# Kernel tuning notes

Hardware: AMD Instinct MI355X
Metric: run time of the kernel (lower is better)

Reference implementation:

```python
import jax, jax.numpy as jnp
from jax import lax
import numpy as np

# ---- module hyper-params (from init_kwargs) ----
ANCHORS = np.array([[42.0, 45.0], [98.0, 130.0], [180.0, 260.0],
                    [300.0, 180.0], [400.0, 400.0]], dtype=np.float32)  # (A,2) pixels
STRIDE = 32
NUM_CLASSES = 80
A = ANCHORS.shape[0]
IMG_H, IMG_W = 1024, 1024  # decode img_size
BN_EPS = 1e-5
TW_CLAMP_MAX = 8.0


def setup_inputs() -> dict:
    key = jax.random.key(0)
    ks = jax.random.split(key, 8)
    B, Cin, S = 32, 512, 32
    Cout = A * (5 + NUM_CLASSES)  # 425
    return {
        "features": jax.random.normal(ks[0], (B, Cin, S, S), jnp.float32),
        "conv1_w": jax.random.normal(ks[1], (1024, Cin, 3, 3), jnp.float32) * 0.02,
        "bn_gamma": jax.random.uniform(ks[2], (1024,), jnp.float32, 0.5, 1.5),
        "bn_beta": jax.random.normal(ks[3], (1024,), jnp.float32) * 0.1,
        "bn_mean": jax.random.normal(ks[4], (1024,), jnp.float32) * 0.1,
        "bn_var": jax.random.uniform(ks[5], (1024,), jnp.float32, 0.5, 1.5),
        "conv2_w": jax.random.normal(ks[6], (Cout, 1024, 1, 1), jnp.float32) * 0.02,
        "conv2_b": jax.random.normal(ks[7], (Cout,), jnp.float32) * 0.02,
    }


def _conv_pred(features, conv1_w, bn_gamma, bn_beta, bn_mean, bn_var, conv2_w, conv2_b):
    dn = ("NCHW", "OIHW", "NCHW")
    x = lax.conv_general_dilated(features, conv1_w, (1, 1), ((1, 1), (1, 1)),
                                 dimension_numbers=dn)
    # BatchNorm (eval mode) fused with LeakyReLU(0.1)
    scale = bn_gamma / jnp.sqrt(bn_var + BN_EPS)
    x = x * scale[None, :, None, None] + (bn_beta - bn_mean * scale)[None, :, None, None]
    x = jnp.where(x > 0, x, 0.1 * x)
    p = lax.conv_general_dilated(x, conv2_w, (1, 1), ((0, 0), (0, 0)),
                                 dimension_numbers=dn)
    p = p + conv2_b[None, :, None, None]
    # (B, A*(5+C), Sy, Sx) -> (B, Sy, Sx, A*(5+C))
    return jnp.transpose(p, (0, 2, 3, 1))


def _decode(preds):
    B, Sy, Sx, _ = preds.shape
    C = NUM_CLASSES
    p = preds.reshape(B, Sy, Sx, A, 5 + C)
    tx, ty, tw, th, to = p[..., 0], p[..., 1], p[..., 2], p[..., 3], p[..., 4]
    cls_logits = p[..., 5:]

    bx = jax.nn.sigmoid(tx)
    by = jax.nn.sigmoid(ty)
    bw = jnp.exp(jnp.minimum(tw, TW_CLAMP_MAX))
    bh = jnp.exp(jnp.minimum(th, TW_CLAMP_MAX))
    obj = jax.nn.sigmoid(to)
    cls_prob = jax.nn.softmax(cls_logits, axis=-1)

    grid_y = jnp.arange(Sy, dtype=preds.dtype)[None, :, None, None]  # (1,Sy,1,1)
    grid_x = jnp.arange(Sx, dtype=preds.dtype)[None, None, :, None]  # (1,1,Sx,1)
    anc = jnp.asarray(ANCHORS) / STRIDE  # cell units
    anc_w = anc[:, 0][None, None, None, :]
    anc_h = anc[:, 1][None, None, None, :]

    cx = (bx + grid_x) * STRIDE
    cy = (by + grid_y) * STRIDE
    pw = anc_w * bw * STRIDE
    ph = anc_h * bh * STRIDE

    x1 = jnp.clip(cx - pw * 0.5, 0.0, IMG_W - 1)
    y1 = jnp.clip(cy - ph * 0.5, 0.0, IMG_H - 1)
    x2 = jnp.clip(cx + pw * 0.5, 0.0, IMG_W - 1)
    y2 = jnp.clip(cy + ph * 0.5, 0.0, IMG_H - 1)

    boxes = jnp.stack((x1, y1, x2, y2), axis=-1).reshape(B, -1, 4)  # (B, Sy*Sx*A, 4)
    scores = (obj * jnp.max(cls_prob, axis=-1)).reshape(B, -1)       # (B, Sy*Sx*A)
    labels = jnp.argmax(cls_prob, axis=-1).reshape(B, -1)            # (B, Sy*Sx*A)
    out5 = jnp.concatenate([boxes, scores[..., None]], axis=-1)      # (B, N, 5)
    return out5, labels


def reference(features, conv1_w, bn_gamma, bn_beta, bn_mean, bn_var, conv2_w, conv2_b):
    preds = _conv_pred(features, conv1_w, bn_gamma, bn_beta, bn_mean, bn_var,
                       conv2_w, conv2_b)
    out5, labels = _decode(preds)
    return out5, labels
```

## Files before the change

### kernel.cpp

```cpp
#include <hip/hip_runtime.h>


typedef _Float16 f16;
typedef _Float16 f16x8 __attribute__((ext_vector_type(8)));
typedef _Float16 f16x4v __attribute__((ext_vector_type(4)));
typedef float    f32x4 __attribute__((ext_vector_type(4)));

__device__ __forceinline__ void gload16(const f16* g, f16* l) {
  __builtin_amdgcn_global_load_lds(
      (const __attribute__((address_space(1))) void*)g,
      (__attribute__((address_space(3))) void*)l, 16, 0, 0);
}

#define MFMA(a, b, c) __builtin_amdgcn_mfma_f32_16x16x32_f16(a, b, c, 0, 0, 0)
#define ASM_VMCNT(N) asm volatile("s_waitcnt vmcnt(" #N ")" ::: "memory")
#define SBAR()                           \
  {                                      \
    __builtin_amdgcn_s_barrier();        \
    __builtin_amdgcn_sched_barrier(0);   \
  }

#define R_AH 0
#define R_AL 16384
#define R_BH 32768
#define R_BL 49152

__device__ const float c_AW[5] = {42.f, 98.f, 180.f, 300.f, 400.f};
__device__ const float c_AH_[5] = {45.f, 130.f, 260.f, 180.f, 400.f};

__global__ void prep_misc(const float* __restrict__ g, const float* __restrict__ be,
                          const float* __restrict__ mn, const float* __restrict__ vr,
                          const float* __restrict__ b2,
                          float* __restrict__ scale, float* __restrict__ shift,
                          float* __restrict__ bias) {
  int i = threadIdx.x;
  float s = g[i] / sqrtf(vr[i] + 1e-5f);
  shift[i] = be[i] - mn[i] * s;
  scale[i] = s * (1.0f / 1024.0f);
  if (i < 512) bias[i] = (i < 425) ? b2[i] : 0.f;
}

__global__ __launch_bounds__(256) void prep_w1(const float* __restrict__ w,
                                               f16* __restrict__ Ah, f16* __restrict__ Al) {
  const int co = blockIdx.x;
  const int k = blockIdx.y * 256 + threadIdx.x;
  const int ky = k / 1536, rem = k - ky * 1536;
  const int kx = rem >> 9, ci = rem & 511;
  float v = w[((co * 512 + ci) * 3 + ky) * 3 + kx] * 1024.f;
  f16 h = (f16)v;
  Ah[(long)co * 4608 + k] = h;
  Al[(long)co * 4608 + k] = (f16)(v - (float)h);
}

__global__ __launch_bounds__(256) void prep_w2(const float* __restrict__ w,
                                               f16* __restrict__ Ah, f16* __restrict__ Al) {
  const int co = blockIdx.x;
  const int ci = blockIdx.y * 256 + threadIdx.x;
  float v = (co < 425) ? w[co * 1024 + ci] * 1024.f : 0.f;
  f16 h = (f16)v;
  Ah[co * 1024 + ci] = h;
  Al[co * 1024 + ci] = (f16)(v - (float)h);
}

__global__ __launch_bounds__(256) void prep_feat(const float* __restrict__ f,
                                                 f16* __restrict__ fph, f16* __restrict__ fpl) {
  __shared__ float lds[256][33];
  const int y = blockIdx.x, b = blockIdx.y, t = threadIdx.x;
  const int xx = t & 31, cig = t >> 5;
  const float* src = f + ((long)b * 512) * 1024 + y * 32;

  for (int half = 0; half < 2; ++half) {
    const int cibase = half * 256;
    for (int rep = 0; rep < 32; ++rep) {
      int ci = rep * 8 + cig;
      lds[ci][xx] = src[(long)(cibase + ci) * 1024 + xx];
    }
    __syncthreads();
    const long rowbase = ((long)(b * 34) + (y + 1)) * 34 + 1;
    for (int xp = 0; xp < 32; ++xp) {
      float v = lds[t][xp];
      f16 h = (f16)v;
      long o = (rowbase + xp) * 512 + cibase + t;
      fph[o] = h;
      fpl[o] = (f16)(v - (float)h);
    }
    __syncthreads();
  }
}

__global__ __launch_bounds__(512, 2) void gemm1(
    const f16* __restrict__ A1h, const f16* __restrict__ A1l,
    const f16* __restrict__ Bh, const f16* __restrict__ Bl,
    const float* __restrict__ scale, const float* __restrict__ shift,
    f16* __restrict__ xth, f16* __restrict__ xtl) {
  __shared__ __align__(16) f16 S[65536];
  const int tid = threadIdx.x;
  const int l = tid & 63, w = tid >> 6;
  const int wm = w >> 2, wn = w & 3;
  const int rho = l & 15, cq = l >> 4;
  const int sc = (cq - rho) & 3;
  const int roff = (rho + 16 * ((cq + rho) & 3)) * 8;
  const int nt = blockIdx.x, mt = blockIdx.y;
  const int n0 = nt * 256, co0 = mt * 256;
  const int b = n0 >> 10, y0 = (n0 & 1023) >> 5;

  const int a0u = (w & 3) + (w >> 2) * 8;
  const int a1u = a0u + 4;
  const int b0u = (w & 1) + (w >> 1) * 4;
  const int b1u = b0u + 2;

  const long aS0 = (long)(co0 + a0u * 16 + rho) * 4608 + sc * 8;
  const long aS1 = (long)(co0 + a1u * 16 + rho) * 4608 + sc * 8;
  const int c0 = b0u * 16 + rho, c1 = b1u * 16 + rho;
  const long bS0 = ((long)(b * 34 + y0 + (c0 >> 5)) * 34 + (c0 & 31)) * 512 + sc * 8;
  const long bS1 = ((long)(b * 34 + y0 + (c1 >> 5)) * 34 + (c1 & 31)) * 512 + sc * 8;

  f32x4 acc[8][4] = {};
  f16x8 ah[4], al[4], bh[2], bl[2];

  gload16(A1h + aS0, &S[R_AH + a0u * 512]);
  gload16(A1l + aS0, &S[R_AL + a0u * 512]);
  gload16(Bh + bS0, &S[R_BH + b0u * 512]);
  gload16(Bl + bS0, &S[R_BL + b0u * 512]);
  gload16(A1h + aS1, &S[R_AH + a1u * 512]);
  gload16(A1l + aS1, &S[R_AL + a1u * 512]);
  gload16(Bh + bS1, &S[R_BH + b1u * 512]);
  gload16(Bl + bS1, &S[R_BL + b1u * 512]);
  ASM_VMCNT(4);
  SBAR();

  for (int t = 0; t < 144; ++t) {
    const int cb = (t & 1) << 13;
    const int nb = 8192 - cb;
    const int s1 = (t < 143) ? t + 1 : t;
    const int ky1 = s1 / 48, r1 = s1 - ky1 * 48;
    const int kx1 = r1 >> 4, ci1 = (r1 & 15) << 5;
    const long kAn = (long)s1 * 32;
    const long kBn = (long)(ky1 * 34 + kx1) * 512 + ci1;

#pragma unroll
    for (int mf = 0; mf < 4; ++mf) {
      const int u = wm * 8 + mf;
      ah[mf] = *(const f16x8*)&S[R_AH + cb + u * 512 + roff];
      al[mf] = *(const f16x8*)&S[R_AL + cb + u * 512 + roff];
    }
#pragma unroll
    for (int nf = 0; nf < 2; ++nf) {
      const int u = wn * 4 + nf;
      bh[nf] = *(const f16x8*)&S[R_BH + cb + u * 512 + roff];
      bl[nf] = *(const f16x8*)&S[R_BL + cb + u * 512 + roff];
    }
    gload16(A1h + aS0 + kAn, &S[R_AH + nb + a0u * 512]);
    gload16(A1l + aS0 + kAn, &S[R_AL + nb + a0u * 512]);
    ASM_VMCNT(2);
    SBAR();
    __builtin_amdgcn_s_setprio(1);
#pragma unroll
    for (int mf = 0; mf < 4; ++mf)
#pragma unroll
      for (int nf = 0; nf < 2; ++nf) {
        acc[mf][nf] = MFMA(ah[mf], bh[nf], acc[mf][nf]);
        acc[mf][nf] = MFMA(ah[mf], bl[nf], acc[mf][nf]);
        acc[mf][nf] = MFMA(al[mf], bh[nf], acc[mf][nf]);
      }
    __builtin_amdgcn_s_setprio(0);
    SBAR();

#pragma unroll
    for (int nf = 0; nf < 2; ++nf) {
      const int u = wn * 4 + 2 + nf;
      bh[nf] = *(const f16x8*)&S[R_BH + cb + u * 512 + roff];
      bl[nf] = *(const f16x8*)&S[R_BL + cb + u * 512 + roff];
    }
    gload16(Bh + bS0 + kBn, &S[R_BH + nb + b0u * 512]);
    gload16(Bl + bS0 + kBn, &S[R_BL + nb + b0u * 512]);
    SBAR();
    __builtin_amdgcn_s_setprio(1);
#pragma unroll
    for (int mf = 0; mf < 4; ++mf)
#pragma unroll
      for (int nf = 0; nf < 2; ++nf) {
        acc[mf][2 + nf] = MFMA(ah[mf], bh[nf], acc[mf][2 + nf]);
        acc[mf][2 + nf] = MFMA(ah[mf], bl[nf], acc[mf][2 + nf]);
        acc[mf][2 + nf] = MFMA(al[mf], bh[nf], acc[mf][2 + nf]);
      }
    __builtin_amdgcn_s_setprio(0);
    SBAR();

#pragma unroll
    for (int mf = 0; mf < 4; ++mf) {
      const int u = wm * 8 + 4 + mf;
      ah[mf] = *(const f16x8*)&S[R_AH + cb + u * 512 + roff];
      al[mf] = *(const f16x8*)&S[R_AL + cb + u * 512 + roff];
    }
#pragma unroll
    for (int nf = 0; nf < 2; ++nf) {
      const int u = wn * 4 + nf;
      bh[nf] = *(const f16x8*)&S[R_BH + cb + u * 512 + roff];
      bl[nf] = *(const f16x8*)&S[R_BL + cb + u * 512 + roff];
    }
    gload16(A1h + aS1 + kAn, &S[R_AH + nb + a1u * 512]);
    gload16(A1l + aS1 + kAn, &S[R_AL + nb + a1u * 512]);
    SBAR();
    __builtin_amdgcn_s_setprio(1);
#pragma unroll
    for (int mf = 0; mf < 4; ++mf)
#pragma unroll
      for (int nf = 0; nf < 2; ++nf) {
        acc[4 + mf][nf] = MFMA(ah[mf], bh[nf], acc[4 + mf][nf]);
        acc[4 + mf][nf] = MFMA(ah[mf], bl[nf], acc[4 + mf][nf]);
        acc[4 + mf][nf] = MFMA(al[mf], bh[nf], acc[4 + mf][nf]);
      }
    __builtin_amdgcn_s_setprio(0);
    SBAR();

#pragma unroll
    for (int nf = 0; nf < 2; ++nf) {
      const int u = wn * 4 + 2 + nf;
      bh[nf] = *(const f16x8*)&S[R_BH + cb + u * 512 + roff];
      bl[nf] = *(const f16x8*)&S[R_BL + cb + u * 512 + roff];
    }
    gload16(Bh + bS1 + kBn, &S[R_BH + nb + b1u * 512]);
    gload16(Bl + bS1 + kBn, &S[R_BL + nb + b1u * 512]);
    ASM_VMCNT(4);
    SBAR();
    __builtin_amdgcn_s_setprio(1);
#pragma unroll
    for (int mf = 0; mf < 4; ++mf)
#pragma unroll
      for (int nf = 0; nf < 2; ++nf) {
        acc[4 + mf][2 + nf] = MFMA(ah[mf], bh[nf], acc[4 + mf][2 + nf]);
        acc[4 + mf][2 + nf] = MFMA(ah[mf], bl[nf], acc[4 + mf][2 + nf]);
        acc[4 + mf][2 + nf] = MFMA(al[mf], bh[nf], acc[4 + mf][2 + nf]);
      }
    __builtin_amdgcn_s_setprio(0);
    SBAR();
  }

#pragma unroll
  for (int am = 0; am < 8; ++am) {
    const int cob = co0 + wm * 128 + am * 16 + cq * 4;
    const float4 scv = *(const float4*)(scale + cob);
    const float4 shv = *(const float4*)(shift + cob);
#pragma unroll
    for (int an = 0; an < 4; ++an) {
      const int col = n0 + wn * 64 + an * 16 + rho;
      f32x4 a = acc[am][an];
      float v0 = a[0] * scv.x + shv.x; v0 = v0 > 0.f ? v0 : 0.1f * v0;
      float v1 = a[1] * scv.y + shv.y; v1 = v1 > 0.f ? v1 : 0.1f * v1;
      float v2 = a[2] * scv.z + shv.z; v2 = v2 > 0.f ? v2 : 0.1f * v2;
      float v3 = a[3] * scv.w + shv.w; v3 = v3 > 0.f ? v3 : 0.1f * v3;
      f16 h0 = (f16)v0, h1 = (f16)v1, h2 = (f16)v2, h3 = (f16)v3;
      f16x4v hv = {h0, h1, h2, h3};
      f16x4v lv = {(f16)(v0 - (float)h0), (f16)(v1 - (float)h1),
                   (f16)(v2 - (float)h2), (f16)(v3 - (float)h3)};
      *(f16x4v*)(xth + (long)col * 1024 + cob) = hv;
      *(f16x4v*)(xtl + (long)col * 1024 + cob) = lv;
    }
  }
}

__global__ __launch_bounds__(512, 2) void gemm2(
    const f16* __restrict__ A2h, const f16* __restrict__ A2l,
    const f16* __restrict__ Bh, const f16* __restrict__ Bl,
    const float* __restrict__ bias, float* __restrict__ preds) {
  __shared__ __align__(16) f16 S[65536];
  const int tid = threadIdx.x;
  const int l = tid & 63, w = tid >> 6;
  const int wm = w >> 2, wn = w & 3;
  const int rho = l & 15, cq = l >> 4;
  const int sc = (cq - rho) & 3;
  const int roff = (rho + 16 * ((cq + rho) & 3)) * 8;
  const int nt = blockIdx.x, mt = blockIdx.y;
  const int n0 = nt * 256, co0 = mt * 256;

  const int a0u = (w & 3) + (w >> 2) * 8;
  const int a1u = a0u + 4;
  const int b0u = (w & 1) + (w >> 1) * 4;
  const int b1u = b0u + 2;

  const long aS0 = (long)(co0 + a0u * 16 + rho) * 1024 + sc * 8;
  const long aS1 = (long)(co0 + a1u * 16 + rho) * 1024 + sc * 8;
  const long bS0 = (long)(n0 + b0u * 16 + rho) * 1024 + sc * 8;
  const long bS1 = (long)(n0 + b1u * 16 + rho) * 1024 + sc * 8;

  f32x4 acc[8][4] = {};
  f16x8 ah[4], al[4], bh[2], bl[2];

  gload16(A2h + aS0, &S[R_AH + a0u * 512]);
  gload16(A2l + aS0, &S[R_AL + a0u * 512]);
  gload16(Bh + bS0, &S[R_BH + b0u * 512]);
  gload16(Bl + bS0, &S[R_BL + b0u * 512]);
  gload16(A2h + aS1, &S[R_AH + a1u * 512]);
  gload16(A2l + aS1, &S[R_AL + a1u * 512]);
  gload16(Bh + bS1, &S[R_BH + b1u * 512]);
  gload16(Bl + bS1, &S[R_BL + b1u * 512]);
  ASM_VMCNT(4);
  SBAR();

  for (int t = 0; t < 32; ++t) {
    const int cb = (t & 1) << 13;
    const int nb = 8192 - cb;
    const long kn = (long)((t < 31) ? t + 1 : t) * 32;

#pragma unroll
    for (int mf = 0; mf < 4; ++mf) {
      const int u = wm * 8 + mf;
      ah[mf] = *(const f16x8*)&S[R_AH + cb + u * 512 + roff];
      al[mf] = *(const f16x8*)&S[R_AL + cb + u * 512 + roff];
    }
#pragma unroll
    for (int nf = 0; nf < 2; ++nf) {
      const int u = wn * 4 + nf;
      bh[nf] = *(const f16x8*)&S[R_BH + cb + u * 512 + roff];
      bl[nf] = *(const f16x8*)&S[R_BL + cb + u * 512 + roff];
    }
    gload16(A2h + aS0 + kn, &S[R_AH + nb + a0u * 512]);
    gload16(A2l + aS0 + kn, &S[R_AL + nb + a0u * 512]);
    ASM_VMCNT(2);
    SBAR();
    __builtin_amdgcn_s_setprio(1);
#pragma unroll
    for (int mf = 0; mf < 4; ++mf)
#pragma unroll
      for (int nf = 0; nf < 2; ++nf) {
        acc[mf][nf] = MFMA(ah[mf], bh[nf], acc[mf][nf]);
        acc[mf][nf] = MFMA(ah[mf], bl[nf], acc[mf][nf]);
        acc[mf][nf] = MFMA(al[mf], bh[nf], acc[mf][nf]);
      }
    __builtin_amdgcn_s_setprio(0);
    SBAR();

#pragma unroll
    for (int nf = 0; nf < 2; ++nf) {
      const int u = wn * 4 + 2 + nf;
      bh[nf] = *(const f16x8*)&S[R_BH + cb + u * 512 + roff];
      bl[nf] = *(const f16x8*)&S[R_BL + cb + u * 512 + roff];
    }
    gload16(Bh + bS0 + kn, &S[R_BH + nb + b0u * 512]);
    gload16(Bl + bS0 + kn, &S[R_BL + nb + b0u * 512]);
    SBAR();
    __builtin_amdgcn_s_setprio(1);
#pragma unroll
    for (int mf = 0; mf < 4; ++mf)
#pragma unroll
      for (int nf = 0; nf < 2; ++nf) {
        acc[mf][2 + nf] = MFMA(ah[mf], bh[nf], acc[mf][2 + nf]);
        acc[mf][2 + nf] = MFMA(ah[mf], bl[nf], acc[mf][2 + nf]);
        acc[mf][2 + nf] = MFMA(al[mf], bh[nf], acc[mf][2 + nf]);
      }
    __builtin_amdgcn_s_setprio(0);
    SBAR();

#pragma unroll
    for (int mf = 0; mf < 4; ++mf) {
      const int u = wm * 8 + 4 + mf;
      ah[mf] = *(const f16x8*)&S[R_AH + cb + u * 512 + roff];
      al[mf] = *(const f16x8*)&S[R_AL + cb + u * 512 + roff];
    }
#pragma unroll
    for (int nf = 0; nf < 2; ++nf) {
      const int u = wn * 4 + nf;
      bh[nf] = *(const f16x8*)&S[R_BH + cb + u * 512 + roff];
      bl[nf] = *(const f16x8*)&S[R_BL + cb + u * 512 + roff];
    }
    gload16(A2h + aS1 + kn, &S[R_AH + nb + a1u * 512]);
    gload16(A2l + aS1 + kn, &S[R_AL + nb + a1u * 512]);
    SBAR();
    __builtin_amdgcn_s_setprio(1);
#pragma unroll
    for (int mf = 0; mf < 4; ++mf)
#pragma unroll
      for (int nf = 0; nf < 2; ++nf) {
        acc[4 + mf][nf] = MFMA(ah[mf], bh[nf], acc[4 + mf][nf]);
        acc[4 + mf][nf] = MFMA(ah[mf], bl[nf], acc[4 + mf][nf]);
        acc[4 + mf][nf] = MFMA(al[mf], bh[nf], acc[4 + mf][nf]);
      }
    __builtin_amdgcn_s_setprio(0);
    SBAR();

#pragma unroll
    for (int nf = 0; nf < 2; ++nf) {
      const int u = wn * 4 + 2 + nf;
      bh[nf] = *(const f16x8*)&S[R_BH + cb + u * 512 + roff];
      bl[nf] = *(const f16x8*)&S[R_BL + cb + u * 512 + roff];
    }
    gload16(Bh + bS1 + kn, &S[R_BH + nb + b1u * 512]);
    gload16(Bl + bS1 + kn, &S[R_BL + nb + b1u * 512]);
    ASM_VMCNT(4);
    SBAR();
    __builtin_amdgcn_s_setprio(1);
#pragma unroll
    for (int mf = 0; mf < 4; ++mf)
#pragma unroll
      for (int nf = 0; nf < 2; ++nf) {
        acc[4 + mf][2 + nf] = MFMA(ah[mf], bh[nf], acc[4 + mf][2 + nf]);
        acc[4 + mf][2 + nf] = MFMA(ah[mf], bl[nf], acc[4 + mf][2 + nf]);
        acc[4 + mf][2 + nf] = MFMA(al[mf], bh[nf], acc[4 + mf][2 + nf]);
      }
    __builtin_amdgcn_s_setprio(0);
    SBAR();
  }

#pragma unroll
  for (int am = 0; am < 8; ++am) {
    const int cob = co0 + wm * 128 + am * 16 + cq * 4;
    const float4 bi = *(const float4*)(bias + cob);
#pragma unroll
    for (int an = 0; an < 4; ++an) {
      const int col = n0 + wn * 64 + an * 16 + rho;
      f32x4 a = acc[am][an];
      float4 o;
      o.x = a[0] * 9.765625e-4f + bi.x;
      o.y = a[1] * 9.765625e-4f + bi.y;
      o.z = a[2] * 9.765625e-4f + bi.z;
      o.w = a[3] * 9.765625e-4f + bi.w;
      *(float4*)(preds + (long)col * 512 + cob) = o;
    }
  }
}

__global__ __launch_bounds__(256) void decode(const float* __restrict__ preds,
                                              float* __restrict__ out) {
  const int t = blockIdx.x * 256 + threadIdx.x;
  const int b = t / 5120, rem = t % 5120, pos = rem / 5, a = rem % 5;
  const int n = (b << 10) + pos;
  const float* p = preds + (long)n * 512 + a * 85;

  float tx = p[0], ty = p[1], tw = p[2], th = p[3], to = p[4];
  float mx = p[5];
  int arg = 0;
  for (int i = 1; i < 80; ++i) {
    float v = p[5 + i];
    if (v > mx) { mx = v; arg = i; }
  }
  float sum = 0.f;
  for (int i = 0; i < 80; ++i) sum += expf(p[5 + i] - mx);

  float obj = 1.f / (1.f + expf(-to));
  float score = obj / sum;
  float bx = 1.f / (1.f + expf(-tx));
  float by = 1.f / (1.f + expf(-ty));
  float bw = expf(fminf(tw, 8.f));
  float bh2 = expf(fminf(th, 8.f));
  float cx = (bx + (float)(pos & 31)) * 32.f;
  float cy = (by + (float)(pos >> 5)) * 32.f;
  float pw = c_AW[a] * bw;
  float ph = c_AH_[a] * bh2;
  float x1 = fminf(fmaxf(cx - 0.5f * pw, 0.f), 1023.f);
  float y1 = fminf(fmaxf(cy - 0.5f * ph, 0.f), 1023.f);
  float x2 = fminf(fmaxf(cx + 0.5f * pw, 0.f), 1023.f);
  float y2 = fminf(fmaxf(cy + 0.5f * ph, 0.f), 1023.f);

  const long o = ((long)b * 5120 + pos * 5 + a) * 5;
  out[o + 0] = x1;
  out[o + 1] = y1;
  out[o + 2] = x2;
  out[o + 3] = y2;
  out[o + 4] = score;
  out[819200 + (long)b * 5120 + pos * 5 + a] = (float)arg;
}

extern "C" void kernel_launch(void* const* d_in, const int* in_sizes, int n_in,
                              void* d_out, int out_size, void* d_ws, size_t ws_size,
                              hipStream_t stream) {
  (void)in_sizes; (void)n_in; (void)out_size; (void)ws_size;
  const float* features = (const float*)d_in[0];
  const float* conv1_w = (const float*)d_in[1];
  const float* bn_g = (const float*)d_in[2];
  const float* bn_b = (const float*)d_in[3];
  const float* bn_m = (const float*)d_in[4];
  const float* bn_v = (const float*)d_in[5];
  const float* conv2_w = (const float*)d_in[6];
  const float* conv2_b = (const float*)d_in[7];
  float* out = (float*)d_out;
  char* ws = (char*)d_ws;

  f16* fph = (f16*)(ws + 0);
  f16* fpl = (f16*)(ws + 37879808L);
  f16* A1h = (f16*)(ws + 75759616L);
  f16* A1l = (f16*)(ws + 85196800L);
  f16* A2h = (f16*)(ws + 94633984L);
  f16* A2l = (f16*)(ws + 95682560L);
  float* scale = (float*)(ws + 96731136L);
  float* shift = (float*)(ws + 96735232L);
  float* bias = (float*)(ws + 96739328L);
  f16* xth = (f16*)(ws + 96741376L);
  f16* xtl = (f16*)(ws + 163850240L);
  float* preds = (float*)(ws + 0);

  hipMemsetAsync(ws, 0, 75759616L, stream);
  prep_misc<<<1, 1024, 0, stream>>>(bn_g, bn_b, bn_m, bn_v, conv2_b, scale, shift, bias);
  prep_w1<<<dim3(1024, 18), 256, 0, stream>>>(conv1_w, A1h, A1l);
  prep_w2<<<dim3(512, 4), 256, 0, stream>>>(conv2_w, A2h, A2l);
  prep_feat<<<dim3(32, 32), 256, 0, stream>>>(features, fph, fpl);
  gemm1<<<dim3(128, 4), 512, 0, stream>>>(A1h, A1l, fph, fpl, scale, shift, xth, xtl);
  gemm2<<<dim3(128, 2), 512, 0, stream>>>(A2h, A2l, xth, xtl, bias, preds);
  decode<<<640, 256, 0, stream>>>(preds, out);
}
```

Measured before the change: 930.1 us.

## Switch both GEMMs to 32x32x16 MFMA with restructured LDS staging

Both split-f16 GEMM kernels move from 16x16x32 MFMA tiles to 32x32x16 MFMA, with each warp now holding a 4x2 grid of 32x32 accumulators. The LDS tile layout is rebuilt to match: each wave loads a 32-row chunk split into two K-halves, the XOR-style swizzle offsets are dropped, and the pipeline goes from four sub-stages to two per K step. The goal is fewer LDS fragment reads per flop and higher MFMA throughput per instruction. Without the swizzle, LDS bank conflicts may rise, and the epilogue now follows the 32x32 output layout.

Result: slower. 1.148 ms (+23.4%).

```diff
diff --git a/kernel.cpp b/kernel.cpp
--- a/kernel.cpp
+++ b/kernel.cpp
@@ -4,7 +4,7 @@
 typedef _Float16 f16;
 typedef _Float16 f16x8 __attribute__((ext_vector_type(8)));
 typedef _Float16 f16x4v __attribute__((ext_vector_type(4)));
-typedef float    f32x4 __attribute__((ext_vector_type(4)));
+typedef float    f32x16 __attribute__((ext_vector_type(16)));
 
 __device__ __forceinline__ void gload16(const f16* g, f16* l) {
   __builtin_amdgcn_global_load_lds(
@@ -12,7 +12,7 @@
       (__attribute__((address_space(3))) void*)l, 16, 0, 0);
 }
 
-#define MFMA(a, b, c) __builtin_amdgcn_mfma_f32_16x16x32_f16(a, b, c, 0, 0, 0)
+#define MFMA32(a, b, c) __builtin_amdgcn_mfma_f32_32x32x16_f16(a, b, c, 0, 0, 0)
 #define ASM_VMCNT(N) asm volatile("s_waitcnt vmcnt(" #N ")" ::: "memory")
 #define SBAR()                           \
   {                                      \
@@ -97,165 +97,122 @@
   const int tid = threadIdx.x;
   const int l = tid & 63, w = tid >> 6;
   const int wm = w >> 2, wn = w & 3;
-  const int rho = l & 15, cq = l >> 4;
-  const int sc = (cq - rho) & 3;
-  const int roff = (rho + 16 * ((cq + rho) & 3)) * 8;
+  const int l31 = l & 31, lh = l >> 5;
   const int nt = blockIdx.x, mt = blockIdx.y;
   const int n0 = nt * 256, co0 = mt * 256;
   const int b = n0 >> 10, y0 = (n0 & 1023) >> 5;
 
-  const int a0u = (w & 3) + (w >> 2) * 8;
-  const int a1u = a0u + 4;
-  const int b0u = (w & 1) + (w >> 1) * 4;
-  const int b1u = b0u + 2;
-
-  const long aS0 = (long)(co0 + a0u * 16 + rho) * 4608 + sc * 8;
-  const long aS1 = (long)(co0 + a1u * 16 + rho) * 4608 + sc * 8;
-  const int c0 = b0u * 16 + rho, c1 = b1u * 16 + rho;
-  const long bS0 = ((long)(b * 34 + y0 + (c0 >> 5)) * 34 + (c0 & 31)) * 512 + sc * 8;
-  const long bS1 = ((long)(b * 34 + y0 + (c1 >> 5)) * 34 + (c1 & 31)) * 512 + sc * 8;
-
-  f32x4 acc[8][4] = {};
+  const long aSrc = (long)(co0 + 32 * w + l31) * 4608 + 8 * lh;
+  const long bSrc = ((long)(b * 34 + y0 + w) * 34 + l31) * 512 + 8 * lh;
+  const int dA = (w * 2) * 512;
+  const int lro = l * 8;
+
+  f32x16 acc[4][2] = {};
   f16x8 ah[4], al[4], bh[2], bl[2];
 
-  gload16(A1h + aS0, &S[R_AH + a0u * 512]);
-  gload16(A1l + aS0, &S[R_AL + a0u * 512]);
-  gload16(Bh + bS0, &S[R_BH + b0u * 512]);
-  gload16(Bl + bS0, &S[R_BL + b0u * 512]);
-  gload16(A1h + aS1, &S[R_AH + a1u * 512]);
-  gload16(A1l + aS1, &S[R_AL + a1u * 512]);
-  gload16(Bh + bS1, &S[R_BH + b1u * 512]);
-  gload16(Bl + bS1, &S[R_BL + b1u * 512]);
+  gload16(A1h + aSrc, &S[R_AH + dA]);
+  gload16(A1l + aSrc, &S[R_AL + dA]);
+  gload16(Bh + bSrc, &S[R_BH + dA]);
+  gload16(Bl + bSrc, &S[R_BL + dA]);
+  gload16(A1h + aSrc + 16, &S[R_AH + dA + 512]);
+  gload16(A1l + aSrc + 16, &S[R_AL + dA + 512]);
+  gload16(Bh + bSrc + 16, &S[R_BH + dA + 512]);
+  gload16(Bl + bSrc + 16, &S[R_BL + dA + 512]);
   ASM_VMCNT(4);
   SBAR();
 
   for (int t = 0; t < 144; ++t) {
     const int cb = (t & 1) << 13;
     const int nb = 8192 - cb;
-    const int s1 = (t < 143) ? t + 1 : t;
-    const int ky1 = s1 / 48, r1 = s1 - ky1 * 48;
+    const int s1t = (t < 143) ? t + 1 : t;
+    const int ky1 = s1t / 48, r1 = s1t - ky1 * 48;
     const int kx1 = r1 >> 4, ci1 = (r1 & 15) << 5;
-    const long kAn = (long)s1 * 32;
+    const long kAn = (long)s1t * 32;
     const long kBn = (long)(ky1 * 34 + kx1) * 512 + ci1;
 
+    gload16(A1h + aSrc + kAn, &S[R_AH + nb + dA]);
+    gload16(A1l + aSrc + kAn, &S[R_AL + nb + dA]);
+    gload16(Bh + bSrc + kBn, &S[R_BH + nb + dA]);
+    gload16(Bl + bSrc + kBn, &S[R_BL + nb + dA]);
 #pragma unroll
     for (int mf = 0; mf < 4; ++mf) {
-      const int u = wm * 8 + mf;
-      ah[mf] = *(const f16x8*)&S[R_AH + cb + u * 512 + roff];
-      al[mf] = *(const f16x8*)&S[R_AL + cb + u * 512 + roff];
-    }
-#pragma unroll
-    for (int nf = 0; nf < 2; ++nf) {
-      const int u = wn * 4 + nf;
-      bh[nf] = *(const f16x8*)&S[R_BH + cb + u * 512 + roff];
-      bl[nf] = *(const f16x8*)&S[R_BL + cb + u * 512 + roff];
-    }
-    gload16(A1h + aS0 + kAn, &S[R_AH + nb + a0u * 512]);
-    gload16(A1l + aS0 + kAn, &S[R_AL + nb + a0u * 512]);
-    ASM_VMCNT(2);
+      const int ch = ((wm * 4 + mf) * 2) * 512;
+      ah[mf] = *(const f16x8*)&S[R_AH + cb + ch + lro];
+      al[mf] = *(const f16x8*)&S[R_AL + cb + ch + lro];
+    }
+#pragma unroll
+    for (int nf = 0; nf < 2; ++nf) {
+      const int ch = ((wn * 2 + nf) * 2) * 512;
+      bh[nf] = *(const f16x8*)&S[R_BH + cb + ch + lro];
+      bl[nf] = *(const f16x8*)&S[R_BL + cb + ch + lro];
+    }
+    ASM_VMCNT(4);
     SBAR();
     __builtin_amdgcn_s_setprio(1);
 #pragma unroll
     for (int mf = 0; mf < 4; ++mf)
 #pragma unroll
       for (int nf = 0; nf < 2; ++nf) {
-        acc[mf][nf] = MFMA(ah[mf], bh[nf], acc[mf][nf]);
-        acc[mf][nf] = MFMA(ah[mf], bl[nf], acc[mf][nf]);
-        acc[mf][nf] = MFMA(al[mf], bh[nf], acc[mf][nf]);
+        acc[mf][nf] = MFMA32(ah[mf], bh[nf], acc[mf][nf]);
+        acc[mf][nf] = MFMA32(ah[mf], bl[nf], acc[mf][nf]);
+        acc[mf][nf] = MFMA32(al[mf], bh[nf], acc[mf][nf]);
       }
     __builtin_amdgcn_s_setprio(0);
     SBAR();
 
-#pragma unroll
-    for (int nf = 0; nf < 2; ++nf) {
-      const int u = wn * 4 + 2 + nf;
-      bh[nf] = *(const f16x8*)&S[R_BH + cb + u * 512 + roff];
-      bl[nf] = *(const f16x8*)&S[R_BL + cb + u * 512 + roff];
-    }
-    gload16(Bh + bS0 + kBn, &S[R_BH + nb + b0u * 512]);
-    gload16(Bl + bS0 + kBn, &S[R_BL + nb + b0u * 512]);
+    gload16(A1h + aSrc + kAn + 16, &S[R_AH + nb + dA + 512]);
+    gload16(A1l + aSrc + kAn + 16, &S[R_AL + nb + dA + 512]);
+    gload16(Bh + bSrc + kBn + 16, &S[R_BH + nb + dA + 512]);
+    gload16(Bl + bSrc + kBn + 16, &S[R_BL + nb + dA + 512]);
+#pragma unroll
+    for (int mf = 0; mf < 4; ++mf) {
+      const int ch = ((wm * 4 + mf) * 2 + 1) * 512;
+      ah[mf] = *(const f16x8*)&S[R_AH + cb + ch + lro];
+      al[mf] = *(const f16x8*)&S[R_AL + cb + ch + lro];
+    }
+#pragma unroll
+    for (int nf = 0; nf < 2; ++nf) {
+      const int ch = ((wn * 2 + nf) * 2 + 1) * 512;
+      bh[nf] = *(const f16x8*)&S[R_BH + cb + ch + lro];
+      bl[nf] = *(const f16x8*)&S[R_BL + cb + ch + lro];
+    }
+    ASM_VMCNT(4);
     SBAR();
     __builtin_amdgcn_s_setprio(1);
 #pragma unroll
     for (int mf = 0; mf < 4; ++mf)
 #pragma unroll
       for (int nf = 0; nf < 2; ++nf) {
-        acc[mf][2 + nf] = MFMA(ah[mf], bh[nf], acc[mf][2 + nf]);
-        acc[mf][2 + nf] = MFMA(ah[mf], bl[nf], acc[mf][2 + nf]);
-        acc[mf][2 + nf] = MFMA(al[mf], bh[nf], acc[mf][2 + nf]);
+        acc[mf][nf] = MFMA32(ah[mf], bh[nf], acc[mf][nf]);
+        acc[mf][nf] = MFMA32(ah[mf], bl[nf], acc[mf][nf]);
+        acc[mf][nf] = MFMA32(al[mf], bh[nf], acc[mf][nf]);
       }
     __builtin_amdgcn_s_setprio(0);
     SBAR();
-
-#pragma unroll
-    for (int mf = 0; mf < 4; ++mf) {
-      const int u = wm * 8 + 4 + mf;
-      ah[mf] = *(const f16x8*)&S[R_AH + cb + u * 512 + roff];
-      al[mf] = *(const f16x8*)&S[R_AL + cb + u * 512 + roff];
-    }
-#pragma unroll
-    for (int nf = 0; nf < 2; ++nf) {
-      const int u = wn * 4 + nf;
-      bh[nf] = *(const f16x8*)&S[R_BH + cb + u * 512 + roff];
-      bl[nf] = *(const f16x8*)&S[R_BL + cb + u * 512 + roff];
-    }
-    gload16(A1h + aS1 + kAn, &S[R_AH + nb + a1u * 512]);
-    gload16(A1l + aS1 + kAn, &S[R_AL + nb + a1u * 512]);
-    SBAR();
-    __builtin_amdgcn_s_setprio(1);
-#pragma unroll
-    for (int mf = 0; mf < 4; ++mf)
-#pragma unroll
-      for (int nf = 0; nf < 2; ++nf) {
-        acc[4 + mf][nf] = MFMA(ah[mf], bh[nf], acc[4 + mf][nf]);
-        acc[4 + mf][nf] = MFMA(ah[mf], bl[nf], acc[4 + mf][nf]);
-        acc[4 + mf][nf] = MFMA(al[mf], bh[nf], acc[4 + mf][nf]);
-      }
-    __builtin_amdgcn_s_setprio(0);
-    SBAR();
-
-#pragma unroll
-    for (int nf = 0; nf < 2; ++nf) {
-      const int u = wn * 4 + 2 + nf;
-      bh[nf] = *(const f16x8*)&S[R_BH + cb + u * 512 + roff];
-      bl[nf] = *(const f16x8*)&S[R_BL + cb + u * 512 + roff];
-    }
-    gload16(Bh + bS1 + kBn, &S[R_BH + nb + b1u * 512]);
-    gload16(Bl + bS1 + kBn, &S[R_BL + nb + b1u * 512]);
-    ASM_VMCNT(4);
-    SBAR();
-    __builtin_amdgcn_s_setprio(1);
-#pragma unroll
-    for (int mf = 0; mf < 4; ++mf)
-#pragma unroll
-      for (int nf = 0; nf < 2; ++nf) {
-        acc[4 + mf][2 + nf] = MFMA(ah[mf], bh[nf], acc[4 + mf][2 + nf]);
-        acc[4 + mf][2 + nf] = MFMA(ah[mf], bl[nf], acc[4 + mf][2 + nf]);
-        acc[4 + mf][2 + nf] = MFMA(al[mf], bh[nf], acc[4 + mf][2 + nf]);
-      }
-    __builtin_amdgcn_s_setprio(0);
-    SBAR();
-  }
-
-#pragma unroll
-  for (int am = 0; am < 8; ++am) {
-    const int cob = co0 + wm * 128 + am * 16 + cq * 4;
-    const float4 scv = *(const float4*)(scale + cob);
-    const float4 shv = *(const float4*)(shift + cob);
-#pragma unroll
-    for (int an = 0; an < 4; ++an) {
-      const int col = n0 + wn * 64 + an * 16 + rho;
-      f32x4 a = acc[am][an];
-      float v0 = a[0] * scv.x + shv.x; v0 = v0 > 0.f ? v0 : 0.1f * v0;
-      float v1 = a[1] * scv.y + shv.y; v1 = v1 > 0.f ? v1 : 0.1f * v1;
-      float v2 = a[2] * scv.z + shv.z; v2 = v2 > 0.f ? v2 : 0.1f * v2;
-      float v3 = a[3] * scv.w + shv.w; v3 = v3 > 0.f ? v3 : 0.1f * v3;
-      f16 h0 = (f16)v0, h1 = (f16)v1, h2 = (f16)v2, h3 = (f16)v3;
-      f16x4v hv = {h0, h1, h2, h3};
-      f16x4v lv = {(f16)(v0 - (float)h0), (f16)(v1 - (float)h1),
-                   (f16)(v2 - (float)h2), (f16)(v3 - (float)h3)};
-      *(f16x4v*)(xth + (long)col * 1024 + cob) = hv;
-      *(f16x4v*)(xtl + (long)col * 1024 + cob) = lv;
+  }
+
+#pragma unroll
+  for (int mf = 0; mf < 4; ++mf) {
+#pragma unroll
+    for (int nf = 0; nf < 2; ++nf) {
+      const int colB = n0 + wn * 64 + nf * 32 + l31;
+      const long colOff = (long)colB * 1024;
+#pragma unroll
+      for (int rg = 0; rg < 4; ++rg) {
+        const int cob = co0 + wm * 128 + mf * 32 + rg * 8 + lh * 4;
+        const float4 scv = *(const float4*)(scale + cob);
+        const float4 shv = *(const float4*)(shift + cob);
+        float v0 = acc[mf][nf][rg * 4 + 0] * scv.x + shv.x; v0 = v0 > 0.f ? v0 : 0.1f * v0;
+        float v1 = acc[mf][nf][rg * 4 + 1] * scv.y + shv.y; v1 = v1 > 0.f ? v1 : 0.1f * v1;
+        float v2 = acc[mf][nf][rg * 4 + 2] * scv.z + shv.z; v2 = v2 > 0.f ? v2 : 0.1f * v2;
+        float v3 = acc[mf][nf][rg * 4 + 3] * scv.w + shv.w; v3 = v3 > 0.f ? v3 : 0.1f * v3;
+        f16 h0 = (f16)v0, h1 = (f16)v1, h2 = (f16)v2, h3 = (f16)v3;
+        f16x4v hv = {h0, h1, h2, h3};
+        f16x4v lv = {(f16)(v0 - (float)h0), (f16)(v1 - (float)h1),
+                     (f16)(v2 - (float)h2), (f16)(v3 - (float)h3)};
+        *(f16x4v*)(xth + colOff + cob) = hv;
+        *(f16x4v*)(xtl + colOff + cob) = lv;
+      }
     }
   }
 }
@@ -268,33 +225,26 @@
   const int tid = threadIdx.x;
   const int l = tid & 63, w = tid >> 6;
   const int wm = w >> 2, wn = w & 3;
-  const int rho = l & 15, cq = l >> 4;
-  const int sc = (cq - rho) & 3;
-  const int roff = (rho + 16 * ((cq + rho) & 3)) * 8;
+  const int l31 = l & 31, lh = l >> 5;
   const int nt = blockIdx.x, mt = blockIdx.y;
   const int n0 = nt * 256, co0 = mt * 256;
 
-  const int a0u = (w & 3) + (w >> 2) * 8;
-  const int a1u = a0u + 4;
-  const int b0u = (w & 1) + (w >> 1) * 4;
-  const int b1u = b0u + 2;
-
-  const long aS0 = (long)(co0 + a0u * 16 + rho) * 1024 + sc * 8;
-  const long aS1 = (long)(co0 + a1u * 16 + rho) * 1024 + sc * 8;
-  const long bS0 = (long)(n0 + b0u * 16 + rho) * 1024 + sc * 8;
-  const long bS1 = (long)(n0 + b1u * 16 + rho) * 1024 + sc * 8;
-
-  f32x4 acc[8][4] = {};
+  const long aSrc = (long)(co0 + 32 * w + l31) * 1024 + 8 * lh;
+  const long bSrc = (long)(n0 + 32 * w + l31) * 1024 + 8 * lh;
+  const int dA = (w * 2) * 512;
+  const int lro = l * 8;
+
+  f32x16 acc[4][2] = {};
   f16x8 ah[4], al[4], bh[2], bl[2];
 
-  gload16(A2h + aS0, &S[R_AH + a0u * 512]);
-  gload16(A2l + aS0, &S[R_AL + a0u * 512]);
-  gload16(Bh + bS0, &S[R_BH + b0u * 512]);
-  gload16(Bl + bS0, &S[R_BL + b0u * 512]);
-  gload16(A2h + aS1, &S[R_AH + a1u * 512]);
-  gload16(A2l + aS1, &S[R_AL + a1u * 512]);
-  gload16(Bh + bS1, &S[R_BH + b1u * 512]);
-  gload16(Bl + bS1, &S[R_BL + b1u * 512]);
+  gload16(A2h + aSrc, &S[R_AH + dA]);
+  gload16(A2l + aSrc, &S[R_AL + dA]);
+  gload16(Bh + bSrc, &S[R_BH + dA]);
+  gload16(Bl + bSrc, &S[R_BL + dA]);
+  gload16(A2h + aSrc + 16, &S[R_AH + dA + 512]);
+  gload16(A2l + aSrc + 16, &S[R_AL + dA + 512]);
+  gload16(Bh + bSrc + 16, &S[R_BH + dA + 512]);
+  gload16(Bl + bSrc + 16, &S[R_BL + dA + 512]);
   ASM_VMCNT(4);
   SBAR();
 
@@ -303,119 +253,84 @@
     const int nb = 8192 - cb;
     const long kn = (long)((t < 31) ? t + 1 : t) * 32;
 
+    gload16(A2h + aSrc + kn, &S[R_AH + nb + dA]);
+    gload16(A2l + aSrc + kn, &S[R_AL + nb + dA]);
+    gload16(Bh + bSrc + kn, &S[R_BH + nb + dA]);
+    gload16(Bl + bSrc + kn, &S[R_BL + nb + dA]);
 #pragma unroll
     for (int mf = 0; mf < 4; ++mf) {
-      const int u = wm * 8 + mf;
-      ah[mf] = *(const f16x8*)&S[R_AH + cb + u * 512 + roff];
-      al[mf] = *(const f16x8*)&S[R_AL + cb + u * 512 + roff];
-    }
-#pragma unroll
-    for (int nf = 0; nf < 2; ++nf) {
-      const int u = wn * 4 + nf;
-      bh[nf] = *(const f16x8*)&S[R_BH + cb + u * 512 + roff];
-      bl[nf] = *(const f16x8*)&S[R_BL + cb + u * 512 + roff];
-    }
-    gload16(A2h + aS0 + kn, &S[R_AH + nb + a0u * 512]);
-    gload16(A2l + aS0 + kn, &S[R_AL + nb + a0u * 512]);
-    ASM_VMCNT(2);
+      const int ch = ((wm * 4 + mf) * 2) * 512;
+      ah[mf] = *(const f16x8*)&S[R_AH + cb + ch + lro];
+      al[mf] = *(const f16x8*)&S[R_AL + cb + ch + lro];
+    }
+#pragma unroll
+    for (int nf = 0; nf < 2; ++nf) {
+      const int ch = ((wn * 2 + nf) * 2) * 512;
+      bh[nf] = *(const f16x8*)&S[R_BH + cb + ch + lro];
+      bl[nf] = *(const f16x8*)&S[R_BL + cb + ch + lro];
+    }
+    ASM_VMCNT(4);
     SBAR();
     __builtin_amdgcn_s_setprio(1);
 #pragma unroll
     for (int mf = 0; mf < 4; ++mf)
 #pragma unroll
       for (int nf = 0; nf < 2; ++nf) {
-        acc[mf][nf] = MFMA(ah[mf], bh[nf], acc[mf][nf]);
-        acc[mf][nf] = MFMA(ah[mf], bl[nf], acc[mf][nf]);
-        acc[mf][nf] = MFMA(al[mf], bh[nf], acc[mf][nf]);
+        acc[mf][nf] = MFMA32(ah[mf], bh[nf], acc[mf][nf]);
+        acc[mf][nf] = MFMA32(ah[mf], bl[nf], acc[mf][nf]);
+        acc[mf][nf] = MFMA32(al[mf], bh[nf], acc[mf][nf]);
       }
     __builtin_amdgcn_s_setprio(0);
     SBAR();
 
-#pragma unroll
-    for (int nf = 0; nf < 2; ++nf) {
-      const int u = wn * 4 + 2 + nf;
-      bh[nf] = *(const f16x8*)&S[R_BH + cb + u * 512 + roff];
-      bl[nf] = *(const f16x8*)&S[R_BL + cb + u * 512 + roff];
-    }
-    gload16(Bh + bS0 + kn, &S[R_BH + nb + b0u * 512]);
-    gload16(Bl + bS0 + kn, &S[R_BL + nb + b0u * 512]);
+    gload16(A2h + aSrc + kn + 16, &S[R_AH + nb + dA + 512]);
+    gload16(A2l + aSrc + kn + 16, &S[R_AL + nb + dA + 512]);
+    gload16(Bh + bSrc + kn + 16, &S[R_BH + nb + dA + 512]);
+    gload16(Bl + bSrc + kn + 16, &S[R_BL + nb + dA + 512]);
+#pragma unroll
+    for (int mf = 0; mf < 4; ++mf) {
+      const int ch = ((wm * 4 + mf) * 2 + 1) * 512;
+      ah[mf] = *(const f16x8*)&S[R_AH + cb + ch + lro];
+      al[mf] = *(const f16x8*)&S[R_AL + cb + ch + lro];
+    }
+#pragma unroll
+    for (int nf = 0; nf < 2; ++nf) {
+      const int ch = ((wn * 2 + nf) * 2 + 1) * 512;
+      bh[nf] = *(const f16x8*)&S[R_BH + cb + ch + lro];
+      bl[nf] = *(const f16x8*)&S[R_BL + cb + ch + lro];
+    }
+    ASM_VMCNT(4);
     SBAR();
     __builtin_amdgcn_s_setprio(1);
 #pragma unroll
     for (int mf = 0; mf < 4; ++mf)
 #pragma unroll
       for (int nf = 0; nf < 2; ++nf) {
-        acc[mf][2 + nf] = MFMA(ah[mf], bh[nf], acc[mf][2 + nf]);
-        acc[mf][2 + nf] = MFMA(ah[mf], bl[nf], acc[mf][2 + nf]);
-        acc[mf][2 + nf] = MFMA(al[mf], bh[nf], acc[mf][2 + nf]);
+        acc[mf][nf] = MFMA32(ah[mf], bh[nf], acc[mf][nf]);
+        acc[mf][nf] = MFMA32(ah[mf], bl[nf], acc[mf][nf]);
+        acc[mf][nf] = MFMA32(al[mf], bh[nf], acc[mf][nf]);
       }
     __builtin_amdgcn_s_setprio(0);
     SBAR();
-
-#pragma unroll
-    for (int mf = 0; mf < 4; ++mf) {
-      const int u = wm * 8 + 4 + mf;
-      ah[mf] = *(const f16x8*)&S[R_AH + cb + u * 512 + roff];
-      al[mf] = *(const f16x8*)&S[R_AL + cb + u * 512 + roff];
-    }
-#pragma unroll
-    for (int nf = 0; nf < 2; ++nf) {
-      const int u = wn * 4 + nf;
-      bh[nf] = *(const f16x8*)&S[R_BH + cb + u * 512 + roff];
-      bl[nf] = *(const f16x8*)&S[R_BL + cb + u * 512 + roff];
-    }
-    gload16(A2h + aS1 + kn, &S[R_AH + nb + a1u * 512]);
-    gload16(A2l + aS1 + kn, &S[R_AL + nb + a1u * 512]);
-    SBAR();
-    __builtin_amdgcn_s_setprio(1);
-#pragma unroll
-    for (int mf = 0; mf < 4; ++mf)
-#pragma unroll
-      for (int nf = 0; nf < 2; ++nf) {
-        acc[4 + mf][nf] = MFMA(ah[mf], bh[nf], acc[4 + mf][nf]);
-        acc[4 + mf][nf] = MFMA(ah[mf], bl[nf], acc[4 + mf][nf]);
-        acc[4 + mf][nf] = MFMA(al[mf], bh[nf], acc[4 + mf][nf]);
-      }
-    __builtin_amdgcn_s_setprio(0);
-    SBAR();
-
-#pragma unroll
-    for (int nf = 0; nf < 2; ++nf) {
-      const int u = wn * 4 + 2 + nf;
-      bh[nf] = *(const f16x8*)&S[R_BH + cb + u * 512 + roff];
-      bl[nf] = *(const f16x8*)&S[R_BL + cb + u * 512 + roff];
-    }
-    gload16(Bh + bS1 + kn, &S[R_BH + nb + b1u * 512]);
-    gload16(Bl + bS1 + kn, &S[R_BL + nb + b1u * 512]);
-    ASM_VMCNT(4);
-    SBAR();
-    __builtin_amdgcn_s_setprio(1);
-#pragma unroll
-    for (int mf = 0; mf < 4; ++mf)
-#pragma unroll
-      for (int nf = 0; nf < 2; ++nf) {
-        acc[4 + mf][2 + nf] = MFMA(ah[mf], bh[nf], acc[4 + mf][2 + nf]);
-        acc[4 + mf][2 + nf] = MFMA(ah[mf], bl[nf], acc[4 + mf][2 + nf]);
-        acc[4 + mf][2 + nf] = MFMA(al[mf], bh[nf], acc[4 + mf][2 + nf]);
-      }
-    __builtin_amdgcn_s_setprio(0);
-    SBAR();
-  }
-
-#pragma unroll
-  for (int am = 0; am < 8; ++am) {
-    const int cob = co0 + wm * 128 + am * 16 + cq * 4;
-    const float4 bi = *(const float4*)(bias + cob);
-#pragma unroll
-    for (int an = 0; an < 4; ++an) {
-      const int col = n0 + wn * 64 + an * 16 + rho;
-      f32x4 a = acc[am][an];
-      float4 o;
-      o.x = a[0] * 9.765625e-4f + bi.x;
-      o.y = a[1] * 9.765625e-4f + bi.y;
-      o.z = a[2] * 9.765625e-4f + bi.z;
-      o.w = a[3] * 9.765625e-4f + bi.w;
-      *(float4*)(preds + (long)col * 512 + cob) = o;
+  }
+
+#pragma unroll
+  for (int mf = 0; mf < 4; ++mf) {
+#pragma unroll
+    for (int nf = 0; nf < 2; ++nf) {
+      const int colB = n0 + wn * 64 + nf * 32 + l31;
+      const long colOff = (long)colB * 512;
+#pragma unroll
+      for (int rg = 0; rg < 4; ++rg) {
+        const int cob = co0 + wm * 128 + mf * 32 + rg * 8 + lh * 4;
+        const float4 bi = *(const float4*)(bias + cob);
+        float4 o;
+        o.x = acc[mf][nf][rg * 4 + 0] * 9.765625e-4f + bi.x;
+        o.y = acc[mf][nf][rg * 4 + 1] * 9.765625e-4f + bi.y;
+        o.z = acc[mf][nf][rg * 4 + 2] * 9.765625e-4f + bi.z;
+        o.w = acc[mf][nf][rg * 4 + 3] * 9.765625e-4f + bi.w;
+        *(float4*)(preds + colOff + cob) = o;
+      }
     }
   }
 }
```
